# Kernel optimization log

Hardware: AMD Instinct MI355X
Metric: run time of the kernel (lower is better)

Reference implementation:

```python
import jax, jax.numpy as jnp
import numpy as np

B, C, H, W = 4, 128, 64, 64

def setup_inputs() -> dict:
    key = jax.random.key(0)
    ks = jax.random.split(key, 4)
    X = jax.random.normal(ks[0], (B, C, H, W), dtype=jnp.float32)
    Wq = jax.random.normal(ks[1], (C, C), dtype=jnp.float32) * 0.05
    Wk = jax.random.normal(ks[2], (C, C), dtype=jnp.float32) * 0.05
    Wv = jax.random.normal(ks[3], (C, C), dtype=jnp.float32) * 0.05
    bq = jnp.zeros((C,), dtype=jnp.float32)
    bk = jnp.zeros((C,), dtype=jnp.float32)
    bv = jnp.zeros((C,), dtype=jnp.float32)
    return {"X": X, "Wq": Wq, "bq": bq, "Wk": Wk, "bk": bk, "Wv": Wv, "bv": bv}

def reference(X, Wq, bq, Wk, bk, Wv, bv):
    b, c, h, w = X.shape
    hw = h * w
    # 1x1 conv == per-pixel linear over channels
    def proj(Wm, bias):
        y = jnp.einsum('bchw,oc->bohw', X, Wm) + bias[None, :, None, None]
        return y.reshape(b, c, hw).transpose(0, 2, 1)  # (b, hw, c)
    q = proj(Wq, bq)
    k = proj(Wk, bk)
    v = proj(Wv, bv)
    scores = jnp.einsum('bic,bjc->bij', q, k)  # (b, hw_q, hw_k); no 1/sqrt(d)
    # torch Softmax(dim=1) on (b, hw, hw): normalize over the QUERY axis
    a = jax.nn.softmax(scores, axis=1)
    x = jnp.einsum('bij,bjc->bic', a, v)  # (b, hw, c)
    x = x.transpose(0, 2, 1).reshape(b, c, h, w)
    return X + x
```

## Files before the change

kernel.cpp:

```cpp
#include <hip/hip_runtime.h>
#include <hip/hip_bf16.h>


typedef unsigned short u16;
typedef __attribute__((ext_vector_type(8))) __bf16 bf16x8;
typedef __attribute__((ext_vector_type(8))) unsigned short us8;
typedef __attribute__((ext_vector_type(4))) float f32x4;
typedef __attribute__((ext_vector_type(16))) float f32x16;

#define NB 4
#define CH 128
#define NP 4096
#define ISPL 8
#define JSPLF 4
#define JSPLP 8

__device__ __forceinline__ float bf2f(u16 b){ union{float f;unsigned u;}v; v.u=((unsigned)b)<<16; return v.f; }
__device__ __forceinline__ u16 f2bf(float f){ union{float f;unsigned u;}v; v.f=f; unsigned r=v.u + 0x7FFFu + ((v.u>>16)&1u); return (u16)(r>>16); }

__device__ __forceinline__ f32x4 mfma16(bf16x8 a, bf16x8 b, f32x4 c){
  return __builtin_amdgcn_mfma_f32_16x16x32_bf16(a, b, c, 0, 0, 0);
}
__device__ __forceinline__ f32x16 mfma32(bf16x8 a, bf16x8 b, f32x16 c){
  return __builtin_amdgcn_mfma_f32_32x32x16_bf16(a, b, c, 0, 0, 0);
}
__device__ __forceinline__ bf16x8 ld8(const u16* p){
  union { us8 u; bf16x8 b; } v; v.u = *(const us8*)p; return v.b;
}
__device__ __forceinline__ void split8(const float* p, bf16x8& h, bf16x8& l){
  union { us8 u; bf16x8 b; } uh, ul;
  #pragma unroll
  for (int e=0;e<8;++e){
    float f = p[e];
    u16 hb = f2bf(f);
    uh.u[e] = hb;
    ul.u[e] = f2bf(f - bf2f(hb));
  }
  h = uh.b; l = ul.b;
}
__device__ __forceinline__ unsigned pk2(float a, float b){
  float2 f2; f2.x = a; f2.y = b;
  __hip_bfloat162 hb = __float22bfloat162_rn(f2);
  unsigned u; __builtin_memcpy(&u, &hb, 4);
  return u;
}
__device__ __forceinline__ us8 pfrag(const float* p, bool hb1){
  unsigned hA = pk2(p[0], p[1]);
  unsigned hB = pk2(p[2], p[3]);
  unsigned hC = pk2(p[4], p[5]);
  unsigned hD = pk2(p[6], p[7]);
  unsigned s0h = hb1? hA:hC, s1h = hb1? hB:hD;
  unsigned r0h = __shfl_xor(s0h, 32), r1h = __shfl_xor(s1h, 32);
  unsigned dh[4];
  dh[0] = hb1? r0h : hA;  dh[1] = hb1? r1h : hB;
  dh[2] = hb1? hC  : r0h; dh[3] = hb1? hD  : r1h;
  us8 o; __builtin_memcpy(&o, dh, 16); return o;
}
__device__ __forceinline__ void gll16(const void* g, void* l){
  __builtin_amdgcn_global_load_lds((const __attribute__((address_space(1))) void*)g,
                                   (__attribute__((address_space(3))) void*)l, 16, 0, 0);
}

__global__ __launch_bounds__(256) void wsplit_kernel(
    const float* __restrict__ Wq, const float* __restrict__ Wk,
    const float* __restrict__ Wv, u16* __restrict__ Whi, u16* __restrict__ Wlo)
{
  const int m = blockIdx.y;
  const float* W = (m==0) ? Wq : (m==1) ? Wk : Wv;
  int i = blockIdx.x*256 + threadIdx.x;
  float f = W[i];
  u16 hb = f2bf(f);
  Whi[m*CH*CH + i] = hb;
  Wlo[m*CH*CH + i] = f2bf(f - bf2f(hb));
}

__global__ __launch_bounds__(64) void proj_kernel(
    const float* __restrict__ X,
    const u16* __restrict__ Whi, const u16* __restrict__ Wlo,
    const float* __restrict__ bq, const float* __restrict__ bk,
    const float* __restrict__ bv,
    u16* __restrict__ Qhi, u16* __restrict__ Qlo,
    u16* __restrict__ Khi, u16* __restrict__ Klo,
    u16* __restrict__ Vthi, u16* __restrict__ Vtlo)
{
  __shared__ float XT[16][CH+4];
  const int b = blockIdx.y, p0 = blockIdx.x*16, lane = threadIdx.x;
  #pragma unroll
  for (int h=0; h<2; ++h){
    int c = lane + h*64;
    const float* src = X + ((size_t)b*CH + c)*NP + p0;
    #pragma unroll
    for (int v4=0; v4<4; ++v4){
      f32x4 v = *(const f32x4*)(src + v4*4);
      #pragma unroll
      for (int p=0;p<4;++p) XT[v4*4+p][c] = v[p];
    }
  }
  __syncthreads();
  const int l15 = lane&15, quad = lane>>4;
  bf16x8 xh[4], xl[4];
  #pragma unroll
  for (int s=0;s<4;++s) split8(&XT[l15][s*32+quad*8], xh[s], xl[s]);

  const float* bm[2] = {bq, bk};
  u16* OH[2] = {Qhi, Khi};
  u16* OL[2] = {Qlo, Klo};
  #pragma unroll
  for (int m=0;m<2;++m){
    const u16* WH = Whi + m*CH*CH;
    const u16* WL = Wlo + m*CH*CH;
    #pragma unroll
    for (int nt=0;nt<8;++nt){
      f32x4 a = {0.f,0.f,0.f,0.f};
      #pragma unroll
      for (int s=0;s<4;++s){
        size_t g = (size_t)(nt*16+l15)*CH + s*32 + quad*8;
        bf16x8 wh = ld8(&WH[g]), wl = ld8(&WL[g]);
        a = mfma16(xh[s], wl, a);
        a = mfma16(xl[s], wh, a);
        a = mfma16(xh[s], wh, a);
      }
      int o = nt*16 + l15;
      float bias = bm[m][o];
      #pragma unroll
      for (int r=0;r<4;++r){
        int i = p0 + quad*4 + r;
        float q = a[r] + bias;
        u16 hb = f2bf(q);
        size_t idx = ((size_t)b*NP + i)*CH + o;
        OH[m][idx] = hb;
        OL[m][idx] = f2bf(q - bf2f(hb));
      }
    }
  }
  const u16* WH = Whi + 2*CH*CH;
  const u16* WL = Wlo + 2*CH*CH;
  #pragma unroll
  for (int mt=0;mt<8;++mt){
    f32x4 a = {0.f,0.f,0.f,0.f};
    #pragma unroll
    for (int s=0;s<4;++s){
      size_t g = (size_t)(mt*16+l15)*CH + s*32 + quad*8;
      bf16x8 wh = ld8(&WH[g]), wl = ld8(&WL[g]);
      a = mfma16(wh, xl[s], a);
      a = mfma16(wl, xh[s], a);
      a = mfma16(wh, xh[s], a);
    }
    #pragma unroll
    for (int r=0;r<4;++r){
      int co = mt*16 + quad*4 + r;
      float v = a[r] + bv[co];
      u16 hb = f2bf(v);
      size_t idx = ((size_t)b*CH + co)*NP + p0 + l15;
      Vthi[idx] = hb;
      Vtlo[idx] = f2bf(v - bf2f(hb));
    }
  }
}

template<bool STOREP>
__global__ __launch_bounds__(256,3) void stats_kernel(
    const u16* __restrict__ Qhi, const u16* __restrict__ Qlo,
    const u16* __restrict__ Khi, const u16* __restrict__ Klo,
    float* __restrict__ colpart, u16* __restrict__ Pbuf)
{
  __shared__ u16 SQ[2][2][32*CH];
  const int b = blockIdx.z, isplit = blockIdx.y;
  const int tid = threadIdx.x, lane = tid&63, w = tid>>6;
  const int l31 = lane&31, h = lane>>5;
  const int j0w = blockIdx.x*128 + w*32;
  const bool hb1 = (h != 0);

  const int slot0 = w*128 + lane, slot1 = slot0 + 64;
  const int qr0 = slot0&31, qc0 = slot0>>5, qr1 = slot1&31, qc1 = slot1>>5;
  const size_t qg0 = ((size_t)b*NP + qr0)*CH + qc0*8;
  const size_t qg1 = ((size_t)b*NP + qr1)*CH + qc1*8;
  const int lof0 = slot0*8, lof1 = slot1*8;

  bf16x8 kh[8], kl[8];
  #pragma unroll
  for (int ks=0;ks<8;++ks){
    size_t g = ((size_t)b*NP + j0w + l31)*CH + ks*16 + h*8;
    kh[ks] = ld8(&Khi[g]);
    kl[ks] = ld8(&Klo[g]);
  }

  const int ibase = isplit*(NP/ISPL);
  const int NCH = (NP/ISPL)/32;
  const size_t Pjt = ((size_t)(b*128 + blockIdx.x*4 + w))*((size_t)4*NP*8);

  auto stageQ = [&](int t){
    size_t iofs = (size_t)(ibase + t*32)*CH;
    int bf = t&1;
    gll16(&Qhi[qg0 + iofs], &SQ[bf][0][lof0]);
    gll16(&Qhi[qg1 + iofs], &SQ[bf][0][lof1]);
    gll16(&Qlo[qg0 + iofs], &SQ[bf][1][lof0]);
    gll16(&Qlo[qg1 + iofs], &SQ[bf][1][lof1]);
  };
  auto computeS = [&](int t, f32x16& s){
    const u16* Qh = &SQ[t&1][0][0];
    const u16* Ql = &SQ[t&1][1][0];
    #pragma unroll
    for (int r=0;r<16;++r) s[r] = 0.f;
    #pragma unroll
    for (int ks=0;ks<8;++ks){
      int o = (ks*2+h)*256 + l31*8;
      bf16x8 qbh = ld8(&Qh[o]);
      bf16x8 qbl = ld8(&Ql[o]);
      s = mfma32(kh[ks], qbl, s);
      s = mfma32(kl[ks], qbh, s);
      s = mfma32(kh[ks], qbh, s);
    }
  };

  stageQ(0); stageQ(1);
  __syncthreads();
  f32x16 s;
  computeS(0, s);
  __syncthreads();

  float scol[16];
  #pragma unroll
  for (int r=0;r<16;++r) scol[r] = 0.f;

  for (int ic=0; ic<NCH; ++ic){
    if (ic+2 < NCH) stageQ(ic+2);
    float p[16];
    #pragma unroll
    for (int r=0;r<16;++r){ p[r] = __expf(s[r]); scol[r] += p[r]; }
    if (STOREP){
      int iglob = ibase + ic*32 + l31;
      #pragma unroll
      for (int t=0;t<2;++t){
        us8 frag = pfrag(&p[8*t], hb1);
        *(us8*)&Pbuf[Pjt + ((size_t)((t*2+h)*NP) + iglob)*8] = frag;
      }
    }
    if (ic+1 < NCH) computeS(ic+1, s);
    __syncthreads();
  }
  #pragma unroll
  for (int m=1; m<32; m<<=1){
    #pragma unroll
    for (int r=0;r<16;++r) scol[r] += __shfl_xor(scol[r], m);
  }
  if (l31 == 0){
    #pragma unroll
    for (int r=0;r<16;++r){
      int j = j0w + (r&3) + 8*(r>>2) + 4*h;
      colpart[((size_t)(isplit*NB + b))*NP + j] = scol[r];
    }
  }
}

__global__ __launch_bounds__(256) void scalev_kernel(
    u16* __restrict__ Vthi, const u16* __restrict__ Vtlo,
    const float* __restrict__ colpart, u16* __restrict__ Vfrag)
{
  size_t t = (size_t)blockIdx.x*256 + threadIdx.x;
  size_t base = t*8;
  int bc = (int)(base >> 12);
  int b  = bc >> 7;
  int c  = bc & 127;
  int j0 = (int)(base & (NP-1));
  f32x4 s0 = {0.f,0.f,0.f,0.f}, s1 = {0.f,0.f,0.f,0.f};
  #pragma unroll
  for (int k=0;k<ISPL;++k){
    const float* cp = &colpart[((size_t)(k*NB + b))*NP + j0];
    f32x4 a0 = *(const f32x4*)cp;
    f32x4 a1 = *(const f32x4*)(cp+4);
    #pragma unroll
    for (int e=0;e<4;++e){ s0[e]+=a0[e]; s1[e]+=a1[e]; }
  }
  us8 hh = *(const us8*)&Vthi[base];
  us8 ll = *(const us8*)&Vtlo[base];
  us8 oh;
  #pragma unroll
  for (int e=0;e<8;++e){
    float r = 1.0f / (e<4 ? s0[e] : s1[e-4]);
    float v = (bf2f(hh[e]) + bf2f(ll[e])) * r;
    oh[e] = f2bf(v);
  }
  *(us8*)&Vthi[base] = oh;
  if (Vfrag){
    int jt = j0 >> 5;
    int kc = ((j0 >> 4) & 1)*2 + ((j0 >> 3) & 1);
    size_t o = (((size_t)(b*128 + jt))*4 + kc)*((size_t)CH*8) + (size_t)c*8;
    *(us8*)&Vfrag[o] = oh;
  }
}

__global__ __launch_bounds__(256) void copyx_kernel(
    const float* __restrict__ X, float* __restrict__ out)
{
  size_t idx = ((size_t)blockIdx.x*256 + threadIdx.x)*4;
  *(f32x4*)&out[idx] = *(const f32x4*)&X[idx];
}

__global__ __launch_bounds__(256,4) void attnp_kernel(
    const u16* __restrict__ Pbuf, const u16* __restrict__ Vfrag,
    float* __restrict__ xpart)
{
  const int b = blockIdx.z, jsplit = blockIdx.y;
  const int tid = threadIdx.x, lane = tid&63, w = tid>>6;
  const int l31 = lane&31, h = lane>>5;
  const int i0w = blockIdx.x*128 + w*32;

  const int NJT = (NP/JSPLP)/32;

  f32x16 acc[4];
  #pragma unroll
  for (int mt=0;mt<4;++mt)
    #pragma unroll
    for (int r=0;r<16;++r) acc[mt][r] = 0.f;

  for (int jt=0; jt<NJT; ++jt){
    const int jtg = jsplit*NJT + jt;
    const size_t Pjt = ((size_t)(b*128 + jtg))*((size_t)4*NP*8);
    const size_t Vjt = ((size_t)(b*128 + jtg))*((size_t)4*CH*8);
    #pragma unroll
    for (int t=0;t<2;++t){
      bf16x8 Bh = ld8(&Pbuf[Pjt + ((size_t)((t*2+h)*NP) + i0w + l31)*8]);
      #pragma unroll
      for (int mt=0;mt<4;++mt){
        bf16x8 vh = ld8(&Vfrag[Vjt + (size_t)((t*2+h)*CH + mt*32 + l31)*8]);
        acc[mt] = mfma32(vh, Bh, acc[mt]);
      }
    }
  }
  float* xp = xpart + ((size_t)(jsplit*NB + b))*(size_t)CH*NP;
  #pragma unroll
  for (int mt=0;mt<4;++mt){
    #pragma unroll
    for (int r=0;r<16;++r){
      int c = mt*32 + (r&3) + 8*(r>>2) + 4*h;
      xp[(size_t)c*NP + i0w + l31] = acc[mt][r];
    }
  }
}

__global__ __launch_bounds__(256) void final8_kernel(
    const float* __restrict__ X, const float* __restrict__ xpart,
    float* __restrict__ out)
{
  const size_t n = (size_t)NB*CH*NP;
  size_t idx = ((size_t)blockIdx.x*256 + threadIdx.x)*4;
  f32x4 s = *(const f32x4*)&X[idx];
  #pragma unroll
  for (int k=0;k<JSPLP;++k){
    f32x4 p = *(const f32x4*)&xpart[(size_t)k*n + idx];
    #pragma unroll
    for (int e=0;e<4;++e) s[e] += p[e];
  }
  *(f32x4*)&out[idx] = s;
}

__global__ __launch_bounds__(256,2) void attnf_kernel(
    const u16* __restrict__ Qhi, const u16* __restrict__ Qlo,
    const u16* __restrict__ Khi, const u16* __restrict__ Klo,
    const u16* __restrict__ Vthi,
    float* __restrict__ out)
{
  __shared__ u16 SK[2][2][32*CH];
  __shared__ u16 SV[2][4*CH*8];
  const int b = blockIdx.z, jsplit = blockIdx.y;
  const int tid = threadIdx.x, lane = tid&63, w = tid>>6;
  const int l31 = lane&31, h = lane>>5;
  const int i0w = blockIdx.x*128 + w*32;
  const bool hb1 = (h != 0);

  const int slot0 = tid, slot1 = tid + 256;
  const int kr0 = slot0&31, kc0 = slot0>>5, kr1 = slot1&31, kc1 = slot1>>5;
  const size_t kg0 = ((size_t)b*NP + kr0)*CH + kc0*8;
  const size_t kg1 = ((size_t)b*NP + kr1)*CH + kc1*8;
  const size_t vg0 = ((size_t)b*CH + (slot0&127))*NP + (slot0>>7)*8;
  const size_t vg1 = ((size_t)b*CH + (slot1&127))*NP + (slot1>>7)*8;
  const int lof0 = slot0*8, lof1 = slot1*8;

  const int jbase = jsplit*(NP/JSPLF);
  const int NJT = (NP/JSPLF)/32;

  auto stageK = [&](int t){
    size_t jofs = (size_t)(jbase + t*32)*CH;
    int bf = t&1;
    gll16(&Khi[kg0 + jofs], &SK[bf][0][lof0]);
    gll16(&Khi[kg1 + jofs], &SK[bf][0][lof1]);
    gll16(&Klo[kg0 + jofs], &SK[bf][1][lof0]);
    gll16(&Klo[kg1 + jofs], &SK[bf][1][lof1]);
  };
  auto stageV = [&](int t){
    int j0 = jbase + t*32;
    int bf = t&1;
    gll16(&Vthi[vg0 + j0], &SV[bf][lof0]);
    gll16(&Vthi[vg1 + j0], &SV[bf][lof1]);
  };

  bf16x8 qh[8], ql[8];
  #pragma unroll
  for (int ks=0;ks<8;++ks){
    size_t g = ((size_t)b*NP + i0w + l31)*CH + ks*16 + h*8;
    qh[ks] = ld8(&Qhi[g]); ql[ks] = ld8(&Qlo[g]);
  }

  auto computeS = [&](int t, f32x16& s){
    const u16* Kh = &SK[t&1][0][0];
    const u16* Kl = &SK[t&1][1][0];
    #pragma unroll
    for (int r=0;r<16;++r) s[r] = 0.f;
    #pragma unroll
    for (int ks=0;ks<8;++ks){
      int o = (ks*2+h)*256 + l31*8;
      bf16x8 ah = ld8(&Kh[o]);
      bf16x8 al = ld8(&Kl[o]);
      s = mfma32(ah, ql[ks], s);
      s = mfma32(al, qh[ks], s);
      s = mfma32(ah, qh[ks], s);
    }
  };

  f32x16 acc[4];
  #pragma unroll
  for (int mt=0;mt<4;++mt)
    #pragma unroll
    for (int r=0;r<16;++r) acc[mt][r] = 0.f;

  stageK(0); stageV(0); stageK(1);
  __syncthreads();
  f32x16 s;
  computeS(0, s);
  __syncthreads();

  for (int jt=0; jt<NJT; ++jt){
    const int cb = jt&1;
    if (jt+2 < NJT) stageK(jt+2);
    if (jt+1 < NJT) stageV(jt+1);

    float p[16];
    #pragma unroll
    for (int r=0;r<16;++r) p[r] = __expf(s[r]);

    if (jt+1 < NJT) computeS(jt+1, s);

    const u16* Vh = &SV[cb][0];
    #pragma unroll
    for (int t=0;t<2;++t){
      us8 fr = pfrag(&p[8*t], hb1);
      bf16x8 Bh; __builtin_memcpy(&Bh, &fr, 16);
      #pragma unroll
      for (int mt=0;mt<4;++mt){
        int o = (t*2+h)*1024 + (mt*32+l31)*8;
        bf16x8 vh = ld8(&Vh[o]);
        acc[mt] = mfma32(vh, Bh, acc[mt]);
      }
    }
    __syncthreads();
  }
  float* xp = out + (size_t)b*CH*NP;
  #pragma unroll
  for (int mt=0;mt<4;++mt){
    #pragma unroll
    for (int r=0;r<16;++r){
      int c = mt*32 + (r&3) + 8*(r>>2) + 4*h;
      atomicAdd(&xp[(size_t)c*NP + i0w + l31], acc[mt][r]);
    }
  }
}

extern "C" void kernel_launch(void* const* d_in, const int* in_sizes, int n_in,
                              void* d_out, int out_size, void* d_ws, size_t ws_size,
                              hipStream_t stream)
{
  const float* X  = (const float*)d_in[0];
  const float* Wq = (const float*)d_in[1];
  const float* bq = (const float*)d_in[2];
  const float* Wk = (const float*)d_in[3];
  const float* bk = (const float*)d_in[4];
  const float* Wv = (const float*)d_in[5];
  const float* bv = (const float*)d_in[6];
  float* outp = (float*)d_out;

  const size_t n = (size_t)NB*NP*CH;
  u16* Qhi = (u16*)d_ws;
  u16* Qlo = Qhi + n;
  u16* Khi = Qlo + n;
  u16* Klo = Khi + n;
  u16* Vthi = Klo + n;
  u16* Vtlo = Vthi + n;
  u16* Whi  = Vtlo + n;
  u16* Wlo  = Whi + 3*CH*CH;
  float* colpart = (float*)(Wlo + 3*CH*CH);
  u16* Pbuf = (u16*)(colpart + (size_t)ISPL*NB*NP);
  const size_t pelems = (size_t)NB*128*4*NP*8;
  u16* Vfrag = Pbuf + pelems;
  float* xpart = (float*)(Vfrag + n);

  const size_t need = (size_t)((char*)xpart - (char*)d_ws)
                      + (size_t)JSPLP*n*sizeof(float);
  const bool usep = (ws_size >= need);

  wsplit_kernel<<<dim3(CH*CH/256, 3),      256, 0, stream>>>(Wq, Wk, Wv, Whi, Wlo);
  proj_kernel  <<<dim3(NP/16, NB),          64, 0, stream>>>(X, Whi, Wlo, bq, bk, bv,
                                                             Qhi,Qlo, Khi,Klo, Vthi,Vtlo);
  if (usep){
    stats_kernel<true><<<dim3(NP/128, ISPL, NB), 256, 0, stream>>>(
        Qhi,Qlo, Khi,Klo, colpart, Pbuf);
    scalev_kernel<<<dim3(n/(256*8)),       256, 0, stream>>>(Vthi, Vtlo, colpart, Vfrag);
    attnp_kernel <<<dim3(NP/128, JSPLP, NB), 256, 0, stream>>>(Pbuf, Vfrag, xpart);
    final8_kernel<<<dim3(n/(256*4)),       256, 0, stream>>>(X, xpart, outp);
  } else {
    stats_kernel<false><<<dim3(NP/128, ISPL, NB), 256, 0, stream>>>(
        Qhi,Qlo, Khi,Klo, colpart, Pbuf);
    scalev_kernel<<<dim3(n/(256*8)),       256, 0, stream>>>(Vthi, Vtlo, colpart,
                                                             (u16*)nullptr);
    copyx_kernel <<<dim3(n/(256*4)),       256, 0, stream>>>(X, outp);
    attnf_kernel <<<dim3(NP/128, JSPLF, NB), 256, 0, stream>>>(
        Qhi,Qlo, Khi,Klo, Vthi, outp);
  }
}
```

Measured before the change: 226.5 us.

## Store Q in MFMA fragment layout and read it directly in stats kernel

The projection kernel now writes Q in a 32-row fragment-ordered layout when the P-buffer path is used. A new stats kernel reads these fragments straight from global memory, with no LDS staging or block barriers. The query split count is doubled to launch more blocks. The fallback path keeps the row-major Q and a LDS-staged stats kernel without P storage. The trade-off is that the four waves now fetch the same Q through cache instead of sharing one LDS copy, and there are no software prefetches to hide load latency.

```diff
diff --git a/kernel.cpp b/kernel.cpp
--- a/kernel.cpp
+++ b/kernel.cpp
@@ -11,7 +11,7 @@
 #define NB 4
 #define CH 128
 #define NP 4096
-#define ISPL 8
+#define ISPL 16
 #define JSPLF 4
 #define JSPLP 8
 
@@ -79,7 +79,7 @@
     const u16* __restrict__ Whi, const u16* __restrict__ Wlo,
     const float* __restrict__ bq, const float* __restrict__ bk,
     const float* __restrict__ bv,
-    u16* __restrict__ Qhi, u16* __restrict__ Qlo,
+    u16* __restrict__ Qdh, u16* __restrict__ Qdl, int qfrag,
     u16* __restrict__ Khi, u16* __restrict__ Klo,
     u16* __restrict__ Vthi, u16* __restrict__ Vtlo)
 {
@@ -103,8 +103,6 @@
   for (int s=0;s<4;++s) split8(&XT[l15][s*32+quad*8], xh[s], xl[s]);
 
   const float* bm[2] = {bq, bk};
-  u16* OH[2] = {Qhi, Khi};
-  u16* OL[2] = {Qlo, Klo};
   #pragma unroll
   for (int m=0;m<2;++m){
     const u16* WH = Whi + m*CH*CH;
@@ -127,9 +125,20 @@
         int i = p0 + quad*4 + r;
         float q = a[r] + bias;
         u16 hb = f2bf(q);
-        size_t idx = ((size_t)b*NP + i)*CH + o;
-        OH[m][idx] = hb;
-        OL[m][idx] = f2bf(q - bf2f(hb));
+        u16 lb = f2bf(q - bf2f(hb));
+        if (m == 0){
+          if (qfrag){
+            size_t idx = ((size_t)(b*128 + (i>>5))*16 + (o>>3))*256
+                       + (size_t)(i&31)*8 + (o&7);
+            Qdh[idx] = hb; Qdl[idx] = lb;
+          } else {
+            size_t idx = ((size_t)b*NP + i)*CH + o;
+            Qdh[idx] = hb; Qdl[idx] = lb;
+          }
+        } else {
+          size_t idx = ((size_t)b*NP + i)*CH + o;
+          Khi[idx] = hb; Klo[idx] = lb;
+        }
       }
     }
   }
@@ -158,18 +167,82 @@
   }
 }
 
-template<bool STOREP>
-__global__ __launch_bounds__(256,3) void stats_kernel(
+__global__ __launch_bounds__(256,3) void statsb_kernel(
+    const u16* __restrict__ Qfh, const u16* __restrict__ Qfl,
+    const u16* __restrict__ Khi, const u16* __restrict__ Klo,
+    float* __restrict__ colpart, u16* __restrict__ Pbuf)
+{
+  const int b = blockIdx.z, isplit = blockIdx.y;
+  const int tid = threadIdx.x, lane = tid&63, w = tid>>6;
+  const int l31 = lane&31, h = lane>>5;
+  const int j0w = blockIdx.x*128 + w*32;
+  const bool hb1 = (h != 0);
+
+  bf16x8 kh[8], kl[8];
+  #pragma unroll
+  for (int ks=0;ks<8;++ks){
+    size_t g = ((size_t)b*NP + j0w + l31)*CH + ks*16 + h*8;
+    kh[ks] = ld8(&Khi[g]);
+    kl[ks] = ld8(&Klo[g]);
+  }
+
+  const int NCH = (NP/ISPL)/32;
+  const int itbase = isplit*NCH;
+  const size_t Pjt = ((size_t)(b*128 + blockIdx.x*4 + w))*((size_t)4*NP*8);
+
+  float scol[16];
+  #pragma unroll
+  for (int r=0;r<16;++r) scol[r] = 0.f;
+
+  for (int ic=0; ic<NCH; ++ic){
+    const int it = itbase + ic;
+    const size_t qbase = (size_t)(b*128 + it)*(16*256);
+    f32x16 s;
+    #pragma unroll
+    for (int r=0;r<16;++r) s[r] = 0.f;
+    #pragma unroll
+    for (int ks=0;ks<8;++ks){
+      size_t qo = qbase + (size_t)((ks*2+h)*256) + (size_t)l31*8;
+      bf16x8 qbh = ld8(&Qfh[qo]);
+      bf16x8 qbl = ld8(&Qfl[qo]);
+      s = mfma32(kh[ks], qbl, s);
+      s = mfma32(kl[ks], qbh, s);
+      s = mfma32(kh[ks], qbh, s);
+    }
+    float p[16];
+    #pragma unroll
+    for (int r=0;r<16;++r){ p[r] = __expf(s[r]); scol[r] += p[r]; }
+    const int iglob = it*32 + l31;
+    #pragma unroll
+    for (int t=0;t<2;++t){
+      us8 frag = pfrag(&p[8*t], hb1);
+      *(us8*)&Pbuf[Pjt + ((size_t)((t*2+h)*NP) + iglob)*8] = frag;
+    }
+  }
+  #pragma unroll
+  for (int m=1; m<32; m<<=1){
+    #pragma unroll
+    for (int r=0;r<16;++r) scol[r] += __shfl_xor(scol[r], m);
+  }
+  if (l31 == 0){
+    #pragma unroll
+    for (int r=0;r<16;++r){
+      int j = j0w + (r&3) + 8*(r>>2) + 4*h;
+      colpart[((size_t)(isplit*NB + b))*NP + j] = scol[r];
+    }
+  }
+}
+
+__global__ __launch_bounds__(256,3) void statsf_kernel(
     const u16* __restrict__ Qhi, const u16* __restrict__ Qlo,
     const u16* __restrict__ Khi, const u16* __restrict__ Klo,
-    float* __restrict__ colpart, u16* __restrict__ Pbuf)
+    float* __restrict__ colpart)
 {
   __shared__ u16 SQ[2][2][32*CH];
   const int b = blockIdx.z, isplit = blockIdx.y;
   const int tid = threadIdx.x, lane = tid&63, w = tid>>6;
   const int l31 = lane&31, h = lane>>5;
   const int j0w = blockIdx.x*128 + w*32;
-  const bool hb1 = (h != 0);
 
   const int slot0 = w*128 + lane, slot1 = slot0 + 64;
   const int qr0 = slot0&31, qc0 = slot0>>5, qr1 = slot1&31, qc1 = slot1>>5;
@@ -187,7 +260,6 @@
 
   const int ibase = isplit*(NP/ISPL);
   const int NCH = (NP/ISPL)/32;
-  const size_t Pjt = ((size_t)(b*128 + blockIdx.x*4 + w))*((size_t)4*NP*8);
 
   auto stageQ = [&](int t){
     size_t iofs = (size_t)(ibase + t*32)*CH;
@@ -213,7 +285,7 @@
     }
   };
 
-  stageQ(0); stageQ(1);
+  stageQ(0); if (NCH > 1) stageQ(1);
   __syncthreads();
   f32x16 s;
   computeS(0, s);
@@ -225,17 +297,8 @@
 
   for (int ic=0; ic<NCH; ++ic){
     if (ic+2 < NCH) stageQ(ic+2);
-    float p[16];
-    #pragma unroll
-    for (int r=0;r<16;++r){ p[r] = __expf(s[r]); scol[r] += p[r]; }
-    if (STOREP){
-      int iglob = ibase + ic*32 + l31;
-      #pragma unroll
-      for (int t=0;t<2;++t){
-        us8 frag = pfrag(&p[8*t], hb1);
-        *(us8*)&Pbuf[Pjt + ((size_t)((t*2+h)*NP) + iglob)*8] = frag;
-      }
-    }
+    #pragma unroll
+    for (int r=0;r<16;++r) scol[r] += __expf(s[r]);
     if (ic+1 < NCH) computeS(ic+1, s);
     __syncthreads();
   }
@@ -480,9 +543,9 @@
   float* outp = (float*)d_out;
 
   const size_t n = (size_t)NB*NP*CH;
-  u16* Qhi = (u16*)d_ws;
-  u16* Qlo = Qhi + n;
-  u16* Khi = Qlo + n;
+  u16* Qa  = (u16*)d_ws;
+  u16* Qb  = Qa + n;
+  u16* Khi = Qb + n;
   u16* Klo = Khi + n;
   u16* Vthi = Klo + n;
   u16* Vtlo = Vthi + n;
@@ -499,21 +562,22 @@
   const bool usep = (ws_size >= need);
 
   wsplit_kernel<<<dim3(CH*CH/256, 3),      256, 0, stream>>>(Wq, Wk, Wv, Whi, Wlo);
-  proj_kernel  <<<dim3(NP/16, NB),          64, 0, stream>>>(X, Whi, Wlo, bq, bk, bv,
-                                                             Qhi,Qlo, Khi,Klo, Vthi,Vtlo);
+  proj_kernel  <<<dim3(NP/16, NB),          64, 0, stream>>>(
+      X, Whi, Wlo, bq, bk, bv, Qa, Qb, usep ? 1 : 0,
+      Khi, Klo, Vthi, Vtlo);
   if (usep){
-    stats_kernel<true><<<dim3(NP/128, ISPL, NB), 256, 0, stream>>>(
-        Qhi,Qlo, Khi,Klo, colpart, Pbuf);
+    statsb_kernel<<<dim3(NP/128, ISPL, NB), 256, 0, stream>>>(
+        Qa, Qb, Khi, Klo, colpart, Pbuf);
     scalev_kernel<<<dim3(n/(256*8)),       256, 0, stream>>>(Vthi, Vtlo, colpart, Vfrag);
     attnp_kernel <<<dim3(NP/128, JSPLP, NB), 256, 0, stream>>>(Pbuf, Vfrag, xpart);
     final8_kernel<<<dim3(n/(256*4)),       256, 0, stream>>>(X, xpart, outp);
   } else {
-    stats_kernel<false><<<dim3(NP/128, ISPL, NB), 256, 0, stream>>>(
-        Qhi,Qlo, Khi,Klo, colpart, Pbuf);
+    statsf_kernel<<<dim3(NP/128, ISPL, NB), 256, 0, stream>>>(
+        Qa, Qb, Khi, Klo, colpart);
     scalev_kernel<<<dim3(n/(256*8)),       256, 0, stream>>>(Vthi, Vtlo, colpart,
                                                              (u16*)nullptr);
     copyx_kernel <<<dim3(n/(256*4)),       256, 0, stream>>>(X, outp);
     attnf_kernel <<<dim3(NP/128, JSPLF, NB), 256, 0, stream>>>(
-        Qhi,Qlo, Khi,Klo, Vthi, outp);
-  }
-}
+        Qa, Qb, Khi, Klo, Vthi, outp);
+  }
+}
```

Result: slower. 243.3 us (+7.4%).
